# Kernel optimization log

Measured on AMD Instinct MI355X. Metric: run time of the kernel, lower is better.

Reference implementation:

```python
import jax, jax.numpy as jnp
import numpy as np

N_NODES = 50000
N_EDGES = 800000  # undirected edge count E0
D_FEAT = 64
K_STEPS = 10
LAMBDA = 3.0


def setup_inputs() -> dict:
    key = jax.random.key(0)
    k1, k2, k3 = jax.random.split(key, 3)
    x = jax.random.normal(k1, (N_NODES, D_FEAT), dtype=jnp.float32)
    edge_src = jax.random.randint(k2, (N_EDGES,), 0, N_NODES)
    edge_dst = jax.random.randint(k3, (N_EDGES,), 0, N_NODES)
    return {"x": x, "edge_src": edge_src, "edge_dst": edge_dst}


def _forward(x, edge_src, edge_dst):
    N, D = x.shape
    # --- symmetric adjacency (directed edge list, both orientations) ---
    row = jnp.concatenate([edge_src, edge_dst])
    col = jnp.concatenate([edge_dst, edge_src])
    # degree with self loops (fill_diag/add_self_loops weight 1), shared by
    # gcn_norm and inc_norm in the original code
    deg = jax.ops.segment_sum(jnp.ones(row.shape[0], x.dtype), row, num_segments=N) + 1.0
    dis = deg ** -0.5  # deg_inv_sqrt, [N]
    # gcn-normalized adjacency weights D^-1/2 (A+I) D^-1/2
    w = dis[row] * dis[col]          # off-diagonal edge weights [2*E0]
    w_self = dis * dis               # self-loop weights [N]

    def adj_mv(v):  # edge_index @ v
        return jax.ops.segment_sum(w[:, None] * v[col], row, num_segments=N) + w_self[:, None] * v

    # --- normalized incidence matrix (one row per undirected edge) ---
    r = jnp.maximum(edge_src, edge_dst)  # row_index after row>=col mask
    c = jnp.minimum(edge_src, edge_dst)
    a = dis[r]  # +1 entry scaled by deg_inv_sqrt of column r
    b = dis[c]  # -1 entry scaled by deg_inv_sqrt of column c

    def inc_mv(v):  # inc_mat @ v -> [E0, D]
        return a[:, None] * v[r] - b[:, None] * v[c]

    def incT_mv(z):  # inc_mat.t() @ z -> [N, D]
        return (jax.ops.segment_sum(a[:, None] * z, r, num_segments=N)
                - jax.ops.segment_sum(b[:, None] * z, c, num_segments=N))

    def l21_projection(z):
        rn = jnp.linalg.norm(z, axis=1)                 # row L2 norms [E0]
        s = jnp.minimum(rn, LAMBDA)
        s = jnp.where(rn > 0, s / jnp.where(rn > 0, rn, 1.0), s)
        return s[:, None] * z

    hh = x
    z0 = jnp.zeros((edge_src.shape[0], D), x.dtype)

    def step(carry, _):
        xk, zk = carry
        y = 0.25 * hh + 0.75 * adj_mv(xk)
        x_bar = y - 0.25 * incT_mv(zk)
        z_bar = zk + 2.0 * inc_mv(x_bar)
        zk = l21_projection(z_bar)
        xk = y - 0.25 * incT_mv(zk)
        return (xk, zk), None

    (xK, _), _ = jax.lax.scan(step, (x, z0), None, length=K_STEPS)
    return xK


def reference(x, edge_src, edge_dst):
    return _forward(x, edge_src, edge_dst)
```

## Files before the change

kernel.cpp:

```cpp
#include <hip/hip_runtime.h>
#include <hip/hip_fp16.h>
#include <math.h>

constexpr int NN = 50000;
constexpr int NE = 800000;
constexpr int KS = 10;
constexpr float LAM = 3.0f;

constexpr int SCAN_NB = (NN + 255) / 256;
constexpr int NODE_NB = NN * 64 / 256;


__global__ __launch_bounds__(256) void countRC_kernel(
    const int* __restrict__ src, const int* __restrict__ dst,
    int* __restrict__ cR, int* __restrict__ cC) {
  int e = blockIdx.x * 256 + threadIdx.x;
  if (e >= NE) return;
  int s = src[e], d = dst[e];
  int r = s > d ? s : d;
  int c = s > d ? d : s;
  atomicAdd(&cR[r], 1);
  atomicAdd(&cC[c], 1);
}

__global__ __launch_bounds__(256) void dis_kernel(
    const int* __restrict__ cR, const int* __restrict__ cC,
    float* __restrict__ dis) {
  int i = blockIdx.x * 256 + threadIdx.x;
  if (i < NN) dis[i] = 1.0f / sqrtf((float)(cR[i] + cC[i] + 1));
}

__global__ __launch_bounds__(256) void half_copy_kernel(
    const float* __restrict__ X, __half* __restrict__ XH) {
  int i = blockIdx.x * 256 + threadIdx.x;
  if (i >= NN * 16) return;
  float4 v = ((const float4*)X)[i];
  __half2 h0 = __floats2half2_rn(v.x, v.y);
  __half2 h1 = __floats2half2_rn(v.z, v.w);
  uint2 o;
  o.x = *(const unsigned*)&h0;
  o.y = *(const unsigned*)&h1;
  ((uint2*)XH)[i] = o;
}


__global__ __launch_bounds__(256) void scanA_kernel(
    const int* __restrict__ cnt, int* __restrict__ bsum) {
  __shared__ int sm[256];
  int t = threadIdx.x;
  int i = blockIdx.x * 256 + t;
  int v = (i < NN) ? cnt[i] : 0;
  sm[t] = v;
  __syncthreads();
  for (int off = 128; off > 0; off >>= 1) {
    if (t < off) sm[t] += sm[t + off];
    __syncthreads();
  }
  if (t == 0) bsum[blockIdx.x] = sm[0];
}

__global__ __launch_bounds__(256) void scanB_kernel(
    int* __restrict__ bsum, int* __restrict__ boff) {
  __shared__ int sm[256];
  int t = threadIdx.x;
  int v = (t < SCAN_NB) ? bsum[t] : 0;
  sm[t] = v;
  __syncthreads();
  for (int off = 1; off < 256; off <<= 1) {
    int a = (t >= off) ? sm[t - off] : 0;
    __syncthreads();
    sm[t] += a;
    __syncthreads();
  }
  if (t < SCAN_NB) boff[t] = sm[t] - v;
}

__global__ __launch_bounds__(256) void scanC_kernel(
    const int* __restrict__ cnt, const int* __restrict__ boff,
    int* __restrict__ ptr, int* __restrict__ cur) {
  __shared__ int sm[256];
  int t = threadIdx.x;
  int i = blockIdx.x * 256 + t;
  int v = (i < NN) ? cnt[i] : 0;
  sm[t] = v;
  __syncthreads();
  for (int off = 1; off < 256; off <<= 1) {
    int a = (t >= off) ? sm[t - off] : 0;
    __syncthreads();
    sm[t] += a;
    __syncthreads();
  }
  if (i < NN) {
    int ex = boff[blockIdx.x] + sm[t] - v;
    ptr[i] = ex;
    cur[i] = ex;
    if (i == NN - 1) ptr[NN] = ex + v;
  }
}

__global__ __launch_bounds__(256) void sortscatter_kernel(
    const int* __restrict__ src, const int* __restrict__ dst,
    const float* __restrict__ dis,
    int* __restrict__ urR, int* __restrict__ uC,
    int2* __restrict__ cb8, int2* __restrict__ cEnt) {
  int e = blockIdx.x * 256 + threadIdx.x;
  if (e >= NE) return;
  int s = src[e], d = dst[e];
  int r = s > d ? s : d;
  int c = s > d ? d : s;
  int p = atomicAdd(&urR[r], 1);
  cb8[p] = make_int2(c, __float_as_int(dis[c]));
  int q = atomicAdd(&uC[c], 1);
  cEnt[q] = make_int2(r, p);
}

__global__ __launch_bounds__(256) void adjm_kernel(
    const int* __restrict__ rPtr, const int* __restrict__ cPtr,
    const int2* __restrict__ cb8, const int2* __restrict__ cEnt,
    const float* __restrict__ dis, int2* __restrict__ adjM) {
  int w = (int)((blockIdx.x * 256u + threadIdx.x) >> 6);
  if (w >= NN) return;
  int lane = threadIdx.x & 63;
  int rb = rPtr[w], lenR = rPtr[w + 1] - rb;
  int cb = cPtr[w], lenC = cPtr[w + 1] - cb;
  int total = lenR + lenC;
  int ab = rb + cb;
  for (int t = lane; t < total; t += 64) {
    int2 m;
    if (t < lenR) {
      m = cb8[rb + t];
    } else {
      int rr = cEnt[cb + t - lenR].x;
      m = make_int2(rr, __float_as_int(dis[rr]));
    }
    adjM[ab + t] = m;
  }
}


template <int FIRST>
__global__ __launch_bounds__(256) void adj_kernel(
    const __half* __restrict__ XH, const float* __restrict__ H,
    const float* __restrict__ U, const float* __restrict__ dis,
    const int* __restrict__ rPtr, const int* __restrict__ cPtr,
    const int2* __restrict__ adjM,
    float* __restrict__ XB, __half* __restrict__ XBh) {
  int w = (int)((blockIdx.x * 256u + threadIdx.x) >> 6);
  if (w >= NN) return;
  int lane = threadIdx.x & 63;
  int g = lane >> 4, l = lane & 15;
  const uint2* XH2 = (const uint2*)XH;
  int rb = rPtr[w], cb = cPtr[w];
  int ab = rb + cb;
  int total = rPtr[w + 1] + cPtr[w + 1] - ab;
  float ax = 0.f, ay = 0.f, az = 0.f, aw = 0.f;

#define ADJ_ACC(XV, W)                                               \
  {                                                                  \
    float2 p = __half22float2(*(const __half2*)&XV.x);               \
    float2 q = __half22float2(*(const __half2*)&XV.y);               \
    ax = fmaf(W, p.x, ax); ay = fmaf(W, p.y, ay);                    \
    az = fmaf(W, q.x, az); aw = fmaf(W, q.y, aw);                    \
  }

  int t = g;
  for (; t + 12 < total; t += 16) {
    int2 m0 = adjM[ab + t];
    int2 m1 = adjM[ab + t + 4];
    int2 m2 = adjM[ab + t + 8];
    int2 m3 = adjM[ab + t + 12];
    uint2 x0 = XH2[m0.x * 16 + l];
    uint2 x1 = XH2[m1.x * 16 + l];
    uint2 x2 = XH2[m2.x * 16 + l];
    uint2 x3 = XH2[m3.x * 16 + l];
    float w0 = __int_as_float(m0.y), w1 = __int_as_float(m1.y);
    float w2 = __int_as_float(m2.y), w3 = __int_as_float(m3.y);
    ADJ_ACC(x0, w0);
    ADJ_ACC(x1, w1);
    ADJ_ACC(x2, w2);
    ADJ_ACC(x3, w3);
  }
  for (; t < total; t += 4) {
    int2 m0 = adjM[ab + t];
    uint2 x0 = XH2[m0.x * 16 + l];
    float w0 = __int_as_float(m0.y);
    ADJ_ACC(x0, w0);
  }
#undef ADJ_ACC

  ax += __shfl_xor(ax, 16, 64); ay += __shfl_xor(ay, 16, 64);
  az += __shfl_xor(az, 16, 64); aw += __shfl_xor(aw, 16, 64);
  ax += __shfl_xor(ax, 32, 64); ay += __shfl_xor(ay, 32, 64);
  az += __shfl_xor(az, 32, 64); aw += __shfl_xor(aw, 32, 64);
  if (g == 0) {
    float di = dis[w];
    int idx = w * 16 + l;
    uint2 xsu = XH2[idx];
    float2 xsa = __half22float2(*(const __half2*)&xsu.x);
    float2 xsb = __half22float2(*(const __half2*)&xsu.y);
    float4 h4 = ((const float4*)H)[idx];
    float4 y4;
    y4.x = 0.25f * h4.x + 0.75f * di * fmaf(di, xsa.x, ax);
    y4.y = 0.25f * h4.y + 0.75f * di * fmaf(di, xsa.y, ay);
    y4.z = 0.25f * h4.z + 0.75f * di * fmaf(di, xsb.x, az);
    y4.w = 0.25f * h4.w + 0.75f * di * fmaf(di, xsb.y, aw);
    float4 xb;
    if (FIRST) {
      xb = y4;
    } else {
      float4 u4 = ((const float4*)U)[idx];
      xb.x = y4.x - 0.25f * u4.x;
      xb.y = y4.y - 0.25f * u4.y;
      xb.z = y4.z - 0.25f * u4.z;
      xb.w = y4.w - 0.25f * u4.w;
    }
    ((float4*)XB)[idx] = xb;
    __half2 hb0 = __floats2half2_rn(xb.x, xb.y);
    __half2 hb1 = __floats2half2_rn(xb.z, xb.w);
    uint2 ob;
    ob.x = *(const unsigned*)&hb0;
    ob.y = *(const unsigned*)&hb1;
    ((uint2*)XBh)[idx] = ob;
  }
}

template <int FIRST>
__global__ __launch_bounds__(256) void zupd_kernel(
    __half* __restrict__ Z, const __half* __restrict__ XBh,
    const float* __restrict__ dis,
    const int* __restrict__ rPtr, const int2* __restrict__ cb8,
    float* __restrict__ U1) {
  int i = (int)((blockIdx.x * 256u + threadIdx.x) >> 6);
  if (i >= NN) return;
  int w = (i & 1) ? (NN - 1 - (i >> 1)) : (i >> 1);
  int lane = threadIdx.x & 63;
  int g = lane >> 4, l = lane & 15;
  const uint2* X2 = (const uint2*)XBh;
  uint2* Z2 = (uint2*)Z;
  int rb = rPtr[w], re = rPtr[w + 1];
  float a2 = 2.0f * dis[w];
  uint2 xwu = X2[w * 16 + l];
  float2 xwa = __half22float2(*(const __half2*)&xwu.x);
  float2 xwb = __half22float2(*(const __half2*)&xwu.y);
  float tx = a2 * xwa.x, ty = a2 * xwa.y;
  float tz = a2 * xwb.x, tw = a2 * xwb.y;
  float sx = 0.f, sy = 0.f, sz = 0.f, sw = 0.f;

#define Z_PROC(E, CV, XCU, ZU)                                       \
  {                                                                  \
    float b2 = 2.0f * __int_as_float(CV.y);                          \
    float2 xca = __half22float2(*(const __half2*)&XCU.x);            \
    float2 xcb = __half22float2(*(const __half2*)&XCU.y);            \
    float zx, zy, zz, zw;                                            \
    if (FIRST) {                                                     \
      zx = zy = zz = zw = 0.f;                                       \
    } else {                                                         \
      float2 f0 = __half22float2(*(const __half2*)&ZU.x);            \
      float2 f1 = __half22float2(*(const __half2*)&ZU.y);            \
      zx = f0.x; zy = f0.y; zz = f1.x; zw = f1.y;                    \
    }                                                                \
    zx += tx - b2 * xca.x;                                           \
    zy += ty - b2 * xca.y;                                           \
    zz += tz - b2 * xcb.x;                                           \
    zw += tw - b2 * xcb.y;                                           \
    float ss = zx * zx + zy * zy + zz * zz + zw * zw;                \
    ss += __shfl_xor(ss, 1, 64);                                     \
    ss += __shfl_xor(ss, 2, 64);                                     \
    ss += __shfl_xor(ss, 4, 64);                                     \
    ss += __shfl_xor(ss, 8, 64);                                     \
    float rn = sqrtf(ss);                                            \
    float sc = (rn > LAM) ? (LAM / rn) : 1.0f;                       \
    zx *= sc; zy *= sc; zz *= sc; zw *= sc;                          \
    __half2 o0 = __floats2half2_rn(zx, zy);                          \
    __half2 o1 = __floats2half2_rn(zz, zw);                          \
    uint2 outu;                                                      \
    outu.x = *(const unsigned*)&o0;                                  \
    outu.y = *(const unsigned*)&o1;                                  \
    Z2[(E) * 16 + l] = outu;                                         \
    sx += zx; sy += zy; sz += zz; sw += zw;                          \
  }

  int e = rb + g;
  for (; e + 12 < re; e += 16) {
    int2 cv0 = cb8[e];
    int2 cv1 = cb8[e + 4];
    int2 cv2 = cb8[e + 8];
    int2 cv3 = cb8[e + 12];
    uint2 xc0 = X2[cv0.x * 16 + l];
    uint2 xc1 = X2[cv1.x * 16 + l];
    uint2 xc2 = X2[cv2.x * 16 + l];
    uint2 xc3 = X2[cv3.x * 16 + l];
    uint2 zu0, zu1, zu2, zu3;
    if (!FIRST) {
      zu0 = Z2[e * 16 + l];
      zu1 = Z2[(e + 4) * 16 + l];
      zu2 = Z2[(e + 8) * 16 + l];
      zu3 = Z2[(e + 12) * 16 + l];
    }
    Z_PROC(e, cv0, xc0, zu0);
    Z_PROC(e + 4, cv1, xc1, zu1);
    Z_PROC(e + 8, cv2, xc2, zu2);
    Z_PROC(e + 12, cv3, xc3, zu3);
  }
  for (; e < re; e += 4) {
    int2 cv0 = cb8[e];
    uint2 xc0 = X2[cv0.x * 16 + l];
    uint2 zu0;
    if (!FIRST) zu0 = Z2[e * 16 + l];
    Z_PROC(e, cv0, xc0, zu0);
  }
#undef Z_PROC

  sx += __shfl_xor(sx, 16, 64); sy += __shfl_xor(sy, 16, 64);
  sz += __shfl_xor(sz, 16, 64); sw += __shfl_xor(sw, 16, 64);
  sx += __shfl_xor(sx, 32, 64); sy += __shfl_xor(sy, 32, 64);
  sz += __shfl_xor(sz, 32, 64); sw += __shfl_xor(sw, 32, 64);
  if (g == 0) {
    ((float4*)U1)[w * 16 + l] = make_float4(sx, sy, sz, sw);
  }
}

template <int FIRST, int LAST>
__global__ __launch_bounds__(256) void cside_kernel(
    const __half* __restrict__ Z, const float* __restrict__ XB,
    const float* __restrict__ dis,
    const int* __restrict__ cPtr, const int2* __restrict__ cEnt,
    const float* __restrict__ U1, float* __restrict__ U,
    float* __restrict__ Xout, __half* __restrict__ XH) {
  int i = (int)((blockIdx.x * 256u + threadIdx.x) >> 6);
  if (i >= NN) return;
  int w = (i & 1) ? (NN - 1 - (i >> 1)) : (i >> 1);
  int lane = threadIdx.x & 63;
  int g = lane >> 4, l = lane & 15;
  const uint2* Z2 = (const uint2*)Z;
  int cb = cPtr[w], ce = cPtr[w + 1];
  float sx = 0.f, sy = 0.f, sz = 0.f, sw = 0.f;
  int j = cb + g;
  for (; j + 12 < ce; j += 16) {
    int e0 = cEnt[j].y;
    int e1 = cEnt[j + 4].y;
    int e2 = cEnt[j + 8].y;
    int e3 = cEnt[j + 12].y;
    uint2 zu0 = Z2[e0 * 16 + l];
    uint2 zu1 = Z2[e1 * 16 + l];
    uint2 zu2 = Z2[e2 * 16 + l];
    uint2 zu3 = Z2[e3 * 16 + l];
    float2 a0 = __half22float2(*(const __half2*)&zu0.x);
    float2 b0 = __half22float2(*(const __half2*)&zu0.y);
    float2 a1 = __half22float2(*(const __half2*)&zu1.x);
    float2 b1 = __half22float2(*(const __half2*)&zu1.y);
    float2 a2 = __half22float2(*(const __half2*)&zu2.x);
    float2 b2 = __half22float2(*(const __half2*)&zu2.y);
    float2 a3 = __half22float2(*(const __half2*)&zu3.x);
    float2 b3 = __half22float2(*(const __half2*)&zu3.y);
    sx += a0.x + a1.x + a2.x + a3.x;
    sy += a0.y + a1.y + a2.y + a3.y;
    sz += b0.x + b1.x + b2.x + b3.x;
    sw += b0.y + b1.y + b2.y + b3.y;
  }
  for (; j < ce; j += 4) {
    int e0 = cEnt[j].y;
    uint2 zu0 = Z2[e0 * 16 + l];
    float2 a0 = __half22float2(*(const __half2*)&zu0.x);
    float2 b0 = __half22float2(*(const __half2*)&zu0.y);
    sx += a0.x; sy += a0.y; sz += b0.x; sw += b0.y;
  }
  sx += __shfl_xor(sx, 16, 64); sy += __shfl_xor(sy, 16, 64);
  sz += __shfl_xor(sz, 16, 64); sw += __shfl_xor(sw, 16, 64);
  sx += __shfl_xor(sx, 32, 64); sy += __shfl_xor(sy, 32, 64);
  sz += __shfl_xor(sz, 32, 64); sw += __shfl_xor(sw, 32, 64);
  if (g == 0) {
    float di = dis[w];
    int idx = w * 16 + l;
    float4 u1 = ((const float4*)U1)[idx];
    float4 u;
    u.x = di * (u1.x - sx);
    u.y = di * (u1.y - sy);
    u.z = di * (u1.z - sz);
    u.w = di * (u1.w - sw);
    float4 xb = ((const float4*)XB)[idx];
    float4 y4;
    if (FIRST) {
      y4 = xb;
    } else {
      float4 uo = ((const float4*)U)[idx];
      y4.x = xb.x + 0.25f * uo.x;
      y4.y = xb.y + 0.25f * uo.y;
      y4.z = xb.z + 0.25f * uo.z;
      y4.w = xb.w + 0.25f * uo.w;
    }
    float4 o;
    o.x = y4.x - 0.25f * u.x;
    o.y = y4.y - 0.25f * u.y;
    o.z = y4.z - 0.25f * u.z;
    o.w = y4.w - 0.25f * u.w;
    if (LAST) {
      ((float4*)Xout)[idx] = o;
    } else {
      ((float4*)U)[idx] = u;
      __half2 h0 = __floats2half2_rn(o.x, o.y);
      __half2 h1 = __floats2half2_rn(o.z, o.w);
      uint2 oh;
      oh.x = *(const unsigned*)&h0;
      oh.y = *(const unsigned*)&h1;
      ((uint2*)XH)[idx] = oh;
    }
  }
}


extern "C" void kernel_launch(void* const* d_in, const int* in_sizes, int n_in,
                              void* d_out, int out_size, void* d_ws, size_t ws_size,
                              hipStream_t stream) {
  const float* x  = (const float*)d_in[0];
  const int* esrc = (const int*)d_in[1];
  const int* edst = (const int*)d_in[2];
  float* out = (float*)d_out;

  char* base = (char*)d_ws;
  size_t off = 0;
  auto carve = [&](size_t bytes) -> void* {
    void* p = base + off;
    off += (bytes + 255) & ~(size_t)255;
    return p;
  };
  __half* Z   = (__half*)carve((size_t)NE * 64 * 2);
  float* XB   = (float*)carve((size_t)NN * 64 * 4);
  float* U    = (float*)carve((size_t)NN * 64 * 4);
  float* U1   = (float*)carve((size_t)NN * 64 * 4);
  __half* XH  = (__half*)carve((size_t)NN * 64 * 2);
  __half* XBh = (__half*)carve((size_t)NN * 64 * 2);
  float* dis = (float*)carve((size_t)NN * 4);
  int* cR  = (int*)carve((size_t)NN * 4);
  int* cC  = (int*)carve((size_t)NN * 4);
  int* rPtr = (int*)carve((size_t)(NN + 1) * 4);
  int* cPtr = (int*)carve((size_t)(NN + 1) * 4);
  int* urR = (int*)carve((size_t)NN * 4);
  int* uC  = (int*)carve((size_t)NN * 4);
  int* bsum = (int*)carve((size_t)SCAN_NB * 4);
  int* boff = (int*)carve((size_t)SCAN_NB * 4);
  int2* cb8  = (int2*)carve((size_t)(NE + 4) * 8);
  int2* cEnt = (int2*)carve((size_t)(NE + 4) * 8);
  int2* adjM = (int2*)carve((size_t)(2 * NE + 4) * 8);
  (void)ws_size; (void)in_sizes; (void)n_in; (void)out_size;

  hipMemsetAsync(cR, 0, NN * 4, stream);
  hipMemsetAsync(cC, 0, NN * 4, stream);

  const int edgeGrid = (NE + 255) / 256;
  countRC_kernel<<<edgeGrid, 256, 0, stream>>>(esrc, edst, cR, cC);
  dis_kernel<<<(NN + 255) / 256, 256, 0, stream>>>(cR, cC, dis);
  half_copy_kernel<<<(NN * 16 + 255) / 256, 256, 0, stream>>>(x, XH);
  scanA_kernel<<<SCAN_NB, 256, 0, stream>>>(cR, bsum);
  scanB_kernel<<<1, 256, 0, stream>>>(bsum, boff);
  scanC_kernel<<<SCAN_NB, 256, 0, stream>>>(cR, boff, rPtr, urR);
  scanA_kernel<<<SCAN_NB, 256, 0, stream>>>(cC, bsum);
  scanB_kernel<<<1, 256, 0, stream>>>(bsum, boff);
  scanC_kernel<<<SCAN_NB, 256, 0, stream>>>(cC, boff, cPtr, uC);
  sortscatter_kernel<<<edgeGrid, 256, 0, stream>>>(esrc, edst, dis, urR, uC,
                                                   cb8, cEnt);
  adjm_kernel<<<NODE_NB, 256, 0, stream>>>(rPtr, cPtr, cb8, cEnt, dis, adjM);

  for (int k = 0; k < KS; ++k) {
    if (k == 0)
      adj_kernel<1><<<NODE_NB, 256, 0, stream>>>(XH, x, U, dis, rPtr, cPtr,
                                                 adjM, XB, XBh);
    else
      adj_kernel<0><<<NODE_NB, 256, 0, stream>>>(XH, x, U, dis, rPtr, cPtr,
                                                 adjM, XB, XBh);

    if (k == 0)
      zupd_kernel<1><<<NODE_NB, 256, 0, stream>>>(Z, XBh, dis, rPtr, cb8, U1);
    else
      zupd_kernel<0><<<NODE_NB, 256, 0, stream>>>(Z, XBh, dis, rPtr, cb8, U1);

    if (k == 0)
      cside_kernel<1, 0><<<NODE_NB, 256, 0, stream>>>(Z, XB, dis, cPtr, cEnt,
                                                      U1, U, out, XH);
    else if (k == KS - 1)
      cside_kernel<0, 1><<<NODE_NB, 256, 0, stream>>>(Z, XB, dis, cPtr, cEnt,
                                                      U1, U, out, XH);
    else
      cside_kernel<0, 0><<<NODE_NB, 256, 0, stream>>>(Z, XB, dis, cPtr, cEnt,
                                                      U1, U, out, XH);
  }
}
```

Before: 1.377 ms.

## Split half-precision node features into feature halves and store y directly

Node features in fp16 are split into two planes holding the low and high 32 features. The adjacency SpMV grid is doubled so each block gathers only one half, with 8 lanes per neighbour instead of 16. This aims to shrink the gathered working set per plane for better cache hit rates, at the cost of reading every adjacency list twice. The adj kernel also writes y directly, so the cside kernel no longer rebuilds it from XB and the old U, which drops one float4 read per node.

New measurement: 1.484 ms. 7.8% more time.

```diff
diff --git a/kernel.cpp b/kernel.cpp
--- a/kernel.cpp
+++ b/kernel.cpp
@@ -31,7 +31,8 @@
 }
 
 __global__ __launch_bounds__(256) void half_copy_kernel(
-    const float* __restrict__ X, __half* __restrict__ XH) {
+    const float* __restrict__ X, __half* __restrict__ XHlo,
+    __half* __restrict__ XHhi) {
   int i = blockIdx.x * 256 + threadIdx.x;
   if (i >= NN * 16) return;
   float4 v = ((const float4*)X)[i];
@@ -40,7 +41,9 @@
   uint2 o;
   o.x = *(const unsigned*)&h0;
   o.y = *(const unsigned*)&h1;
-  ((uint2*)XH)[i] = o;
+  int w = i >> 4, f4 = i & 15;
+  __half* dst = (f4 < 8) ? XHlo : XHhi;
+  ((uint2*)dst)[w * 8 + (f4 & 7)] = o;
 }
 
 
@@ -140,18 +143,21 @@
 
 template <int FIRST>
 __global__ __launch_bounds__(256) void adj_kernel(
-    const __half* __restrict__ XH, const float* __restrict__ H,
-    const float* __restrict__ U, const float* __restrict__ dis,
+    const __half* __restrict__ XHlo, const __half* __restrict__ XHhi,
+    const float* __restrict__ H, const float* __restrict__ U,
+    const float* __restrict__ dis,
     const int* __restrict__ rPtr, const int* __restrict__ cPtr,
     const int2* __restrict__ adjM,
-    float* __restrict__ XB, __half* __restrict__ XBh) {
-  int w = (int)((blockIdx.x * 256u + threadIdx.x) >> 6);
+    float* __restrict__ Y, __half* __restrict__ XBh) {
+  int bid = blockIdx.x;
+  int half = bid & 1;
+  int nb = bid >> 1;
+  int w = (int)(((unsigned)nb * 256u + threadIdx.x) >> 6);
   if (w >= NN) return;
   int lane = threadIdx.x & 63;
-  int g = lane >> 4, l = lane & 15;
-  const uint2* XH2 = (const uint2*)XH;
-  int rb = rPtr[w], cb = cPtr[w];
-  int ab = rb + cb;
+  int g = lane >> 3, l = lane & 7;
+  const uint2* XH2 = (const uint2*)(half ? XHhi : XHlo);
+  int ab = rPtr[w] + cPtr[w];
   int total = rPtr[w + 1] + cPtr[w + 1] - ab;
   float ax = 0.f, ay = 0.f, az = 0.f, aw = 0.f;
 
@@ -164,38 +170,33 @@
   }
 
   int t = g;
-  for (; t + 12 < total; t += 16) {
+  for (; t + 8 < total; t += 16) {
     int2 m0 = adjM[ab + t];
-    int2 m1 = adjM[ab + t + 4];
-    int2 m2 = adjM[ab + t + 8];
-    int2 m3 = adjM[ab + t + 12];
-    uint2 x0 = XH2[m0.x * 16 + l];
-    uint2 x1 = XH2[m1.x * 16 + l];
-    uint2 x2 = XH2[m2.x * 16 + l];
-    uint2 x3 = XH2[m3.x * 16 + l];
+    int2 m1 = adjM[ab + t + 8];
+    uint2 x0 = XH2[m0.x * 8 + l];
+    uint2 x1 = XH2[m1.x * 8 + l];
     float w0 = __int_as_float(m0.y), w1 = __int_as_float(m1.y);
-    float w2 = __int_as_float(m2.y), w3 = __int_as_float(m3.y);
     ADJ_ACC(x0, w0);
     ADJ_ACC(x1, w1);
-    ADJ_ACC(x2, w2);
-    ADJ_ACC(x3, w3);
-  }
-  for (; t < total; t += 4) {
+  }
+  for (; t < total; t += 8) {
     int2 m0 = adjM[ab + t];
-    uint2 x0 = XH2[m0.x * 16 + l];
+    uint2 x0 = XH2[m0.x * 8 + l];
     float w0 = __int_as_float(m0.y);
     ADJ_ACC(x0, w0);
   }
 #undef ADJ_ACC
 
+  ax += __shfl_xor(ax, 8, 64); ay += __shfl_xor(ay, 8, 64);
+  az += __shfl_xor(az, 8, 64); aw += __shfl_xor(aw, 8, 64);
   ax += __shfl_xor(ax, 16, 64); ay += __shfl_xor(ay, 16, 64);
   az += __shfl_xor(az, 16, 64); aw += __shfl_xor(aw, 16, 64);
   ax += __shfl_xor(ax, 32, 64); ay += __shfl_xor(ay, 32, 64);
   az += __shfl_xor(az, 32, 64); aw += __shfl_xor(aw, 32, 64);
   if (g == 0) {
     float di = dis[w];
-    int idx = w * 16 + l;
-    uint2 xsu = XH2[idx];
+    int idx = w * 16 + half * 8 + l;
+    uint2 xsu = XH2[w * 8 + l];
     float2 xsa = __half22float2(*(const __half2*)&xsu.x);
     float2 xsb = __half22float2(*(const __half2*)&xsu.y);
     float4 h4 = ((const float4*)H)[idx];
@@ -204,6 +205,7 @@
     y4.y = 0.25f * h4.y + 0.75f * di * fmaf(di, xsa.y, ay);
     y4.z = 0.25f * h4.z + 0.75f * di * fmaf(di, xsb.x, az);
     y4.w = 0.25f * h4.w + 0.75f * di * fmaf(di, xsb.y, aw);
+    ((float4*)Y)[idx] = y4;
     float4 xb;
     if (FIRST) {
       xb = y4;
@@ -214,7 +216,6 @@
       xb.z = y4.z - 0.25f * u4.z;
       xb.w = y4.w - 0.25f * u4.w;
     }
-    ((float4*)XB)[idx] = xb;
     __half2 hb0 = __floats2half2_rn(xb.x, xb.y);
     __half2 hb1 = __floats2half2_rn(xb.z, xb.w);
     uint2 ob;
@@ -320,13 +321,14 @@
   }
 }
 
-template <int FIRST, int LAST>
+template <int LAST>
 __global__ __launch_bounds__(256) void cside_kernel(
-    const __half* __restrict__ Z, const float* __restrict__ XB,
+    const __half* __restrict__ Z, const float* __restrict__ Y,
     const float* __restrict__ dis,
     const int* __restrict__ cPtr, const int2* __restrict__ cEnt,
     const float* __restrict__ U1, float* __restrict__ U,
-    float* __restrict__ Xout, __half* __restrict__ XH) {
+    float* __restrict__ Xout, __half* __restrict__ XHlo,
+    __half* __restrict__ XHhi) {
   int i = (int)((blockIdx.x * 256u + threadIdx.x) >> 6);
   if (i >= NN) return;
   int w = (i & 1) ? (NN - 1 - (i >> 1)) : (i >> 1);
@@ -378,17 +380,7 @@
     u.y = di * (u1.y - sy);
     u.z = di * (u1.z - sz);
     u.w = di * (u1.w - sw);
-    float4 xb = ((const float4*)XB)[idx];
-    float4 y4;
-    if (FIRST) {
-      y4 = xb;
-    } else {
-      float4 uo = ((const float4*)U)[idx];
-      y4.x = xb.x + 0.25f * uo.x;
-      y4.y = xb.y + 0.25f * uo.y;
-      y4.z = xb.z + 0.25f * uo.z;
-      y4.w = xb.w + 0.25f * uo.w;
-    }
+    float4 y4 = ((const float4*)Y)[idx];
     float4 o;
     o.x = y4.x - 0.25f * u.x;
     o.y = y4.y - 0.25f * u.y;
@@ -403,7 +395,8 @@
       uint2 oh;
       oh.x = *(const unsigned*)&h0;
       oh.y = *(const unsigned*)&h1;
-      ((uint2*)XH)[idx] = oh;
+      __half* dst = (l < 8) ? XHlo : XHhi;
+      ((uint2*)dst)[w * 8 + (l & 7)] = oh;
     }
   }
 }
@@ -424,12 +417,13 @@
     off += (bytes + 255) & ~(size_t)255;
     return p;
   };
-  __half* Z   = (__half*)carve((size_t)NE * 64 * 2);
-  float* XB   = (float*)carve((size_t)NN * 64 * 4);
-  float* U    = (float*)carve((size_t)NN * 64 * 4);
-  float* U1   = (float*)carve((size_t)NN * 64 * 4);
-  __half* XH  = (__half*)carve((size_t)NN * 64 * 2);
-  __half* XBh = (__half*)carve((size_t)NN * 64 * 2);
+  __half* Z    = (__half*)carve((size_t)NE * 64 * 2);
+  float* Y     = (float*)carve((size_t)NN * 64 * 4);
+  float* U     = (float*)carve((size_t)NN * 64 * 4);
+  float* U1    = (float*)carve((size_t)NN * 64 * 4);
+  __half* XHlo = (__half*)carve((size_t)NN * 32 * 2);
+  __half* XHhi = (__half*)carve((size_t)NN * 32 * 2);
+  __half* XBh  = (__half*)carve((size_t)NN * 64 * 2);
   float* dis = (float*)carve((size_t)NN * 4);
   int* cR  = (int*)carve((size_t)NN * 4);
   int* cC  = (int*)carve((size_t)NN * 4);
@@ -450,7 +444,7 @@
   const int edgeGrid = (NE + 255) / 256;
   countRC_kernel<<<edgeGrid, 256, 0, stream>>>(esrc, edst, cR, cC);
   dis_kernel<<<(NN + 255) / 256, 256, 0, stream>>>(cR, cC, dis);
-  half_copy_kernel<<<(NN * 16 + 255) / 256, 256, 0, stream>>>(x, XH);
+  half_copy_kernel<<<(NN * 16 + 255) / 256, 256, 0, stream>>>(x, XHlo, XHhi);
   scanA_kernel<<<SCAN_NB, 256, 0, stream>>>(cR, bsum);
   scanB_kernel<<<1, 256, 0, stream>>>(bsum, boff);
   scanC_kernel<<<SCAN_NB, 256, 0, stream>>>(cR, boff, rPtr, urR);
@@ -463,25 +457,22 @@
 
   for (int k = 0; k < KS; ++k) {
     if (k == 0)
-      adj_kernel<1><<<NODE_NB, 256, 0, stream>>>(XH, x, U, dis, rPtr, cPtr,
-                                                 adjM, XB, XBh);
+      adj_kernel<1><<<2 * NODE_NB, 256, 0, stream>>>(XHlo, XHhi, x, U, dis,
+                                                     rPtr, cPtr, adjM, Y, XBh);
     else
-      adj_kernel<0><<<NODE_NB, 256, 0, stream>>>(XH, x, U, dis, rPtr, cPtr,
-                                                 adjM, XB, XBh);
+      adj_kernel<0><<<2 * NODE_NB, 256, 0, stream>>>(XHlo, XHhi, x, U, dis,
+                                                     rPtr, cPtr, adjM, Y, XBh);
 
     if (k == 0)
       zupd_kernel<1><<<NODE_NB, 256, 0, stream>>>(Z, XBh, dis, rPtr, cb8, U1);
     else
       zupd_kernel<0><<<NODE_NB, 256, 0, stream>>>(Z, XBh, dis, rPtr, cb8, U1);
 
-    if (k == 0)
-      cside_kernel<1, 0><<<NODE_NB, 256, 0, stream>>>(Z, XB, dis, cPtr, cEnt,
-                                                      U1, U, out, XH);
-    else if (k == KS - 1)
-      cside_kernel<0, 1><<<NODE_NB, 256, 0, stream>>>(Z, XB, dis, cPtr, cEnt,
-                                                      U1, U, out, XH);
+    if (k == KS - 1)
+      cside_kernel<1><<<NODE_NB, 256, 0, stream>>>(Z, Y, dis, cPtr, cEnt,
+                                                   U1, U, out, XHlo, XHhi);
     else
-      cside_kernel<0, 0><<<NODE_NB, 256, 0, stream>>>(Z, XB, dis, cPtr, cEnt,
-                                                      U1, U, out, XH);
-  }
-}
+      cside_kernel<0><<<NODE_NB, 256, 0, stream>>>(Z, Y, dis, cPtr, cEnt,
+                                                   U1, U, out, XHlo, XHhi);
+  }
+}
```
